# Performance work log

Measured on AMD Instinct MI355X. Metric: run time of the kernel, lower is better.

The kernel has to match this reference:

```python
import jax, jax.numpy as jnp
import numpy as np

DIM = 1024
N_SLOTS = 64
SCALE = 1.0 / np.sqrt(DIM).astype(np.float32)


def _orthogonal(key, n, scale):
    a = jax.random.normal(key, (n, n), dtype=jnp.float32)
    q, r = jnp.linalg.qr(a)
    q = q * jnp.sign(jnp.diag(r))[None, :]
    return q * scale


def setup_inputs() -> dict:
    key = jax.random.key(0)
    ks = jax.random.split(key, 8)
    B, T, D = 16, 1024, DIM
    s = 1.0 / np.sqrt(D)
    x = jax.random.normal(ks[0], (B, T, D), dtype=jnp.float32)
    in_proj_w = jax.random.uniform(ks[1], (D, D), minval=-s, maxval=s, dtype=jnp.float32)
    out_proj_w = jax.random.uniform(ks[2], (D, D), minval=-s, maxval=s, dtype=jnp.float32)
    gate_proj_w = jax.random.uniform(ks[3], (D, D), minval=-s, maxval=s, dtype=jnp.float32)
    W_x = jax.random.uniform(ks[4], (D, D), minval=-s, maxval=s, dtype=jnp.float32)
    W_h = _orthogonal(ks[5], D, 0.9)
    W_write = jax.random.uniform(ks[6], (D, D), minval=-s, maxval=s, dtype=jnp.float32)
    b_h = jnp.zeros((D,), dtype=jnp.float32)
    return {"x": x, "in_proj_w": in_proj_w, "out_proj_w": out_proj_w,
            "gate_proj_w": gate_proj_w, "W_x": W_x, "W_h": W_h,
            "W_write": W_write, "b_h": b_h}


def _cell(x_proj, W_x, W_h, W_write, b_h):
    # x_proj: [B, T, D]
    B, T, D = x_proj.shape
    wx_all = jnp.einsum('btd,ed->bte', x_proj, W_x)  # precomputed W_x @ x
    h_tape0 = jnp.zeros((B, N_SLOTS, D), dtype=x_proj.dtype)
    h_work0 = jnp.zeros((B, D), dtype=x_proj.dtype)

    def step(carry, wx_t):
        h_tape, h_work = carry
        Rh = h_work @ W_h.T
        read_attn = jax.nn.softmax(jnp.einsum('bd,bnd->bn', h_work, h_tape) * SCALE, axis=-1)
        read = jnp.einsum('bn,bnd->bd', read_attn, h_tape)
        h_work = jnp.tanh(Rh + wx_t + read + b_h)
        write_val = h_work @ W_write.T
        write_attn = jax.nn.softmax(jnp.einsum('bd,bnd->bn', h_work, h_tape) * SCALE, axis=-1)
        wa = write_attn[..., None]  # [B, N, 1]
        h_tape = (1.0 - wa) * h_tape + wa * write_val[:, None, :]
        return (h_tape, h_work), h_work

    (h_tape_f, h_work_f), h_work_all = jax.lax.scan(
        step, (h_tape0, h_work0), jnp.swapaxes(wx_all, 0, 1))
    return jnp.swapaxes(h_work_all, 0, 1), h_tape_f, h_work_f


def reference(x, in_proj_w, out_proj_w, gate_proj_w, W_x, W_h, W_write, b_h):
    x_proj = x @ in_proj_w.T  # [B, T, D]
    h_work_all, h_tape_f, h_work_f = _cell(x_proj, W_x, W_h, W_write, b_h)
    gate = jax.nn.silu(x @ gate_proj_w.T)
    output = (h_work_all * gate) @ out_proj_w.T
    return output, h_tape_f, h_work_f
```

## Files before the change

kernel.cpp:

```cpp
#include <hip/hip_runtime.h>
#include <math.h>

#define SCALE_F 0.03125f

template<bool BT, int EPI>
__global__ __launch_bounds__(256) void gemm_nt(const float* __restrict__ A,
                                               const float* __restrict__ Bm,
                                               float* __restrict__ C,
                                               int M, int N, int K) {
  __shared__ float As[32][68];
  __shared__ float Bs[32][68];
  const int tid = threadIdx.x;
  const int n0 = blockIdx.x * 64;
  const int m0 = blockIdx.y * 64;
  const int i0 = (tid >> 4) * 4;
  const int j0 = (tid & 15) * 4;
  float acc[4][4] = {};

  for (int k0 = 0; k0 < K; k0 += 32) {
#pragma unroll
    for (int s = 0; s < 2; ++s) {
      int id = tid + 256 * s;
      int r = id >> 3, c4 = id & 7;
      float4 v = *(const float4*)&A[(size_t)(m0 + r) * K + k0 + c4 * 4];
      As[c4 * 4 + 0][r] = v.x; As[c4 * 4 + 1][r] = v.y;
      As[c4 * 4 + 2][r] = v.z; As[c4 * 4 + 3][r] = v.w;
    }
    if (BT) {
#pragma unroll
      for (int s = 0; s < 2; ++s) {
        int id = tid + 256 * s;
        int r = id >> 3, c4 = id & 7;
        float4 v = *(const float4*)&Bm[(size_t)(n0 + r) * K + k0 + c4 * 4];
        Bs[c4 * 4 + 0][r] = v.x; Bs[c4 * 4 + 1][r] = v.y;
        Bs[c4 * 4 + 2][r] = v.z; Bs[c4 * 4 + 3][r] = v.w;
      }
    } else {
#pragma unroll
      for (int s = 0; s < 2; ++s) {
        int id = tid + 256 * s;
        int kk = id >> 4, c4 = id & 15;
        float4 v = *(const float4*)&Bm[(size_t)(k0 + kk) * N + n0 + c4 * 4];
        *(float4*)&Bs[kk][c4 * 4] = v;
      }
    }
    __syncthreads();
#pragma unroll
    for (int kk = 0; kk < 32; ++kk) {
      float4 a = *(const float4*)&As[kk][i0];
      float4 b = *(const float4*)&Bs[kk][j0];
      float av[4] = {a.x, a.y, a.z, a.w};
      float bv[4] = {b.x, b.y, b.z, b.w};
#pragma unroll
      for (int ii = 0; ii < 4; ++ii)
#pragma unroll
        for (int jj = 0; jj < 4; ++jj)
          acc[ii][jj] = fmaf(av[ii], bv[jj], acc[ii][jj]);
    }
    __syncthreads();
  }

#pragma unroll
  for (int ii = 0; ii < 4; ++ii) {
    float4 v;
    float* vp = (float*)&v;
#pragma unroll
    for (int jj = 0; jj < 4; ++jj) {
      float x = acc[ii][jj];
      if (EPI == 1) x = x / (1.0f + __expf(-x));
      vp[jj] = x;
    }
    *(float4*)&C[(size_t)(m0 + i0 + ii) * N + n0 + j0] = v;
  }
}

typedef unsigned long long u64;
__device__ __forceinline__ u64 ald64(const u64* p) {
  return __hip_atomic_load(p, __ATOMIC_RELAXED, __HIP_MEMORY_SCOPE_AGENT);
}
__device__ __forceinline__ void ast64(u64* p, u64 v) {
  __hip_atomic_store(p, v, __ATOMIC_RELAXED, __HIP_MEMORY_SCOPE_AGENT);
}
__device__ __forceinline__ u64 pk(float v, int j) {
  return ((u64)(unsigned)j << 32) | (u64)__float_as_uint(v);
}
__device__ __forceinline__ float pollv(const u64* p, int j) {
  u64 u = ald64(p);
  while ((unsigned)(u >> 32) != (unsigned)j) {
    __builtin_amdgcn_s_sleep(1);
    u = ald64(p);
  }
  return __uint_as_float((unsigned)u);
}

#define TIDX(n, e) ((n) * 64 + (((e) + (n)) & 63))

#define REP32(M) M(0) M(1) M(2) M(3) M(4) M(5) M(6) M(7) M(8) M(9) M(10) \
  M(11) M(12) M(13) M(14) M(15) M(16) M(17) M(18) M(19) M(20) M(21) M(22) \
  M(23) M(24) M(25) M(26) M(27) M(28) M(29) M(30) M(31)

#define RW(i) const float wh##i = Whp[32 * (i)]; \
              const float ww##i = Wwp[32 * (i)];
#define MVI(i) { float4 hh = ht4[cseg + 32 * (i)]; \
  ah0 = fmaf(wh##i, hh.x, ah0); ah1 = fmaf(wh##i, hh.y, ah1); \
  ah2 = fmaf(wh##i, hh.z, ah2); ah3 = fmaf(wh##i, hh.w, ah3); \
  aw0 = fmaf(ww##i, hh.x, aw0); aw1 = fmaf(ww##i, hh.y, aw1); \
  aw2 = fmaf(ww##i, hh.z, aw2); aw3 = fmaf(ww##i, hh.w, aw3); }

__global__ __launch_bounds__(512) void scan_kernel(
    const float* __restrict__ W_h, const float* __restrict__ W_wr,
    const float* __restrict__ b_h, const float* __restrict__ gate,
    float* __restrict__ wx,
    u64* __restrict__ h2,
    u64* __restrict__ ps2,
    u64* __restrict__ Rh2,
    u64* __restrict__ wv2,
    u64* __restrict__ qp2,
    float* __restrict__ hfin,
    float* __restrict__ tape_out)
{
  const int tid  = threadIdx.x;
  const int wg   = blockIdx.x;
  const int g    = wg >> 6;
  const int idx  = wg & 63;
  const int b_loc = idx >> 4;
  const int es   = idx & 15;
  const int gb   = g * 4;
  const int bsel = gb + b_loc;
  const int E0   = es * 64;
  const int R0   = es * 64 + b_loc * 16;
  const int w    = tid >> 6;
  const int lane = tid & 63;
  const int row  = tid >> 5;
  const int cseg = tid & 31;
  const int gr   = R0 + row;
  const int nwr  = tid >> 3;
  const int ksb  = tid & 7;

  __shared__ float h_t[4096];
  __shared__ float tape_l[4096];
  __shared__ float qtmp[16][4];
  __shared__ float ws_lds[64], wa_lds[64], attn_lds[64];
  __shared__ float wv_lds[64], Rh_lds[64], h_own[64], read_lds[64];
  __shared__ volatile float lds_pad[12288];
  lds_pad[tid] = 0.0f; lds_pad[tid + 512] = 0.0f;

  const float* Whp = W_h + (size_t)gr * 1024 + cseg;
  const float* Wwp = W_wr + (size_t)gr * 1024 + cseg;
  REP32(RW)

  const float4* ht4 = (const float4*)h_t;

  for (int i = tid; i < 4096; i += 512) tape_l[i] = 0.0f;

  float bh_r = 0.0f;
  if (w == 0) bh_r = b_h[E0 + lane];
  __syncthreads();

  if (w == 0) {
    size_t xi = (size_t)bsel * 1048576 + E0 + lane;
    float hv = tanhf(wx[xi] + bh_r);
    h_own[lane] = hv;
    ast64(&h2[(size_t)bsel * 1024 + E0 + lane], pk(hv, 1));
    wx[xi] = hv * gate[xi];
  }
  if (tid < 64) ast64(&ps2[(size_t)bsel * 1024 + es * 64 + tid], pk(0.0f, 1));
  __syncthreads();

  for (int j = 1; j <= 1024; ++j) {
    const bool last = (j == 1024);

#pragma unroll
    for (int r = 0; r < 8; ++r) {
      int i = tid + r * 512;
      int bl = i >> 10, d = i & 1023;
      h_t[4 * d + bl] = pollv(&h2[(size_t)(gb + bl) * 1024 + d], j);
    }
    float p0 = pollv(&ps2[(size_t)bsel * 1024 + (ksb * 2) * 64 + nwr], j);
    float p1 = pollv(&ps2[(size_t)bsel * 1024 + (ksb * 2 + 1) * 64 + nwr], j);
    float wxv = 0.0f, gv = 0.0f;
    size_t xj = 0;
    if (w == 0 && !last) {
      xj  = (size_t)bsel * 1048576 + (size_t)j * 1024 + E0 + lane;
      wxv = wx[xj];
      gv  = gate[xj];
    }
    __syncthreads();

    {
      float s = p0 + p1;
      s += __shfl_xor(s, 1);
      s += __shfl_xor(s, 2);
      s += __shfl_xor(s, 4);
      if (ksb == 0) ws_lds[nwr] = s;
    }
    float ah0 = 0.0f, ah1 = 0.0f, ah2 = 0.0f, ah3 = 0.0f;
    float aw0 = 0.0f, aw1 = 0.0f, aw2 = 0.0f, aw3 = 0.0f;
    REP32(MVI)
#pragma unroll
    for (int m = 1; m < 32; m <<= 1) {
      ah0 += __shfl_xor(ah0, m); ah1 += __shfl_xor(ah1, m);
      ah2 += __shfl_xor(ah2, m); ah3 += __shfl_xor(ah3, m);
      aw0 += __shfl_xor(aw0, m); aw1 += __shfl_xor(aw1, m);
      aw2 += __shfl_xor(aw2, m); aw3 += __shfl_xor(aw3, m);
    }
    if (cseg == 0) {
      ast64(&Rh2[(size_t)(gb + 0) * 1024 + gr], pk(ah0, j));
      ast64(&Rh2[(size_t)(gb + 1) * 1024 + gr], pk(ah1, j));
      ast64(&Rh2[(size_t)(gb + 2) * 1024 + gr], pk(ah2, j));
      ast64(&Rh2[(size_t)(gb + 3) * 1024 + gr], pk(ah3, j));
      ast64(&wv2[(size_t)(gb + 0) * 1024 + gr], pk(aw0, j));
      ast64(&wv2[(size_t)(gb + 1) * 1024 + gr], pk(aw1, j));
      ast64(&wv2[(size_t)(gb + 2) * 1024 + gr], pk(aw2, j));
      ast64(&wv2[(size_t)(gb + 3) * 1024 + gr], pk(aw3, j));
      qtmp[row][0] = aw0 * h_t[4 * gr + 0];
      qtmp[row][1] = aw1 * h_t[4 * gr + 1];
      qtmp[row][2] = aw2 * h_t[4 * gr + 2];
      qtmp[row][3] = aw3 * h_t[4 * gr + 3];
    }
    __syncthreads();

    if (w == 0) {
      float s = ws_lds[lane] * SCALE_F;
      float m = s;
#pragma unroll
      for (int off = 1; off < 64; off <<= 1) m = fmaxf(m, __shfl_xor(m, off));
      float ex = __expf(s - m);
      float sum = ex;
#pragma unroll
      for (int off = 1; off < 64; off <<= 1) sum += __shfl_xor(sum, off);
      wa_lds[lane] = ex / sum;
    } else if (w == 1) {
      int bq = lane >> 4, r = lane & 15;
      float s = qtmp[r][bq];
      s += __shfl_xor(s, 1); s += __shfl_xor(s, 2);
      s += __shfl_xor(s, 4); s += __shfl_xor(s, 8);
      if (r == 0) ast64(&qp2[(size_t)(gb + bq) * 64 + idx], pk(s, j));
      float qv = pollv(&qp2[(size_t)bsel * 64 + lane], j);
#pragma unroll
      for (int off = 1; off < 64; off <<= 1) qv += __shfl_xor(qv, off);
      if (!last) {
        float wsr = ws_lds[lane];
        float sm = wsr * SCALE_F;
        float m = sm;
#pragma unroll
        for (int off = 1; off < 64; off <<= 1) m = fmaxf(m, __shfl_xor(m, off));
        float ex = __expf(sm - m);
        float sum = ex;
#pragma unroll
        for (int off = 1; off < 64; off <<= 1) sum += __shfl_xor(sum, off);
        float wa_l = ex / sum;
        float rs = fmaf(wa_l, qv - wsr, wsr) * SCALE_F;
        float m2 = rs;
#pragma unroll
        for (int off = 1; off < 64; off <<= 1) m2 = fmaxf(m2, __shfl_xor(m2, off));
        float ex2 = __expf(rs - m2);
        float sum2 = ex2;
#pragma unroll
        for (int off = 1; off < 64; off <<= 1) sum2 += __shfl_xor(sum2, off);
        attn_lds[lane] = ex2 / sum2;
      }
    } else if (w == 2) {
      wv_lds[lane] = pollv(&wv2[(size_t)bsel * 1024 + E0 + lane], j);
    } else if (w == 3) {
      Rh_lds[lane] = pollv(&Rh2[(size_t)bsel * 1024 + E0 + lane], j);
    }
    __syncthreads();

    {
      float wa = wa_lds[nwr];
#pragma unroll
      for (int i = 0; i < 8; ++i) {
        int e = ksb * 8 + i;
        int ix = TIDX(nwr, e);
        float t = tape_l[ix];
        tape_l[ix] = fmaf(wa, wv_lds[e] - t, t);
      }
    }
    if (last) break;
    __syncthreads();

    {
      int ge = tid >> 3, gn = tid & 7;
      float gsum = 0.0f;
#pragma unroll
      for (int i = 0; i < 8; ++i) {
        int n = gn * 8 + i;
        gsum = fmaf(attn_lds[n], tape_l[TIDX(n, ge)], gsum);
      }
      gsum += __shfl_xor(gsum, 1);
      gsum += __shfl_xor(gsum, 2);
      gsum += __shfl_xor(gsum, 4);
      if (gn == 0) read_lds[ge] = gsum;
    }
    __syncthreads();

    if (w == 0) {
      float hv = tanhf(Rh_lds[lane] + wxv + read_lds[lane] + bh_r);
      h_own[lane] = hv;
      ast64(&h2[(size_t)bsel * 1024 + E0 + lane], pk(hv, j + 1));
      wx[xj] = hv * gv;
    }
    __syncthreads();

    {
      float s = 0.0f;
#pragma unroll
      for (int i = 0; i < 8; ++i) {
        int e = ksb * 8 + i;
        s = fmaf(h_own[e], tape_l[TIDX(nwr, e)], s);
      }
      s += __shfl_xor(s, 1);
      s += __shfl_xor(s, 2);
      s += __shfl_xor(s, 4);
      if (ksb == 0) ast64(&ps2[(size_t)bsel * 1024 + es * 64 + nwr], pk(s, j + 1));
    }
  }

#pragma unroll
  for (int i = 0; i < 8; ++i) {
    int e = ksb * 8 + i;
    tape_out[(size_t)(bsel * 64 + nwr) * 1024 + E0 + e] = tape_l[TIDX(nwr, e)];
  }
  if (w == 0) hfin[(size_t)bsel * 1024 + E0 + lane] = h_own[lane];
}

extern "C" void kernel_launch(void* const* d_in, const int* in_sizes, int n_in,
                              void* d_out, int out_size, void* d_ws, size_t ws_size,
                              hipStream_t stream) {
  (void)in_sizes; (void)n_in; (void)out_size; (void)ws_size;
  const float* x      = (const float*)d_in[0];
  const float* in_w   = (const float*)d_in[1];
  const float* out_w  = (const float*)d_in[2];
  const float* gate_w = (const float*)d_in[3];
  const float* W_x    = (const float*)d_in[4];
  const float* W_h    = (const float*)d_in[5];
  const float* W_wr   = (const float*)d_in[6];
  const float* b_h    = (const float*)d_in[7];

  float* out  = (float*)d_out;
  float* tape = out + (size_t)16 * 1024 * 1024;
  float* hfin = tape + (size_t)16 * 64 * 1024;

  float* ws = (float*)d_ws;
  u64* h2  = (u64*)ws;
  u64* ps2 = (u64*)(ws + 32768);
  u64* Rh2 = (u64*)(ws + 65536);
  u64* wv2 = (u64*)(ws + 98304);
  u64* qp2 = (u64*)(ws + 131072);
  float* M1 = ws;
  float* wx = ws + (1 << 20);

  float* gate = out;

  dim3 blk(256);
  gemm_nt<false, 0><<<dim3(16, 16), blk, 0, stream>>>(W_x, in_w, M1, 1024, 1024, 1024);
  gemm_nt<true, 1><<<dim3(16, 256), blk, 0, stream>>>(x, gate_w, gate, 16384, 1024, 1024);
  gemm_nt<true, 0><<<dim3(16, 256), blk, 0, stream>>>(x, M1, wx, 16384, 1024, 1024);
  hipMemsetAsync(ws, 0, 133120 * sizeof(float), stream);
  scan_kernel<<<256, 512, 0, stream>>>(W_h, W_wr, b_h, gate, wx, h2, ps2,
                                       Rh2, wv2, qp2, hfin, tape);
  gemm_nt<true, 0><<<dim3(16, 256), blk, 0, stream>>>(wx, out_w, out, 16384, 1024, 1024);
}
```

Measured before the change: 10.94 ms.

## Batch spin-poll loads and publish per-wave q partials to cut sync latency

Each thread's per-step polling of h and partial-score flags becomes one combined loop that issues all ten tagged loads together and retries only when some tag is stale. Before, eight separate poll loops ran one after another. The q partial products are now reduced per wave with shuffles and published directly to a larger global buffer (8 entries per workgroup). This removes the LDS qtmp staging, the extra reduction, and the serial publish-then-poll step inside wave 1, and wave 1 now polls 8 entries per lane. The cost is more global atomic traffic and a larger memset region.

Result: slower. 12.69 ms (+15.9%).

```diff
diff --git a/kernel.cpp b/kernel.cpp
--- a/kernel.cpp
+++ b/kernel.cpp
@@ -84,13 +84,16 @@
 __device__ __forceinline__ u64 pk(float v, int j) {
   return ((u64)(unsigned)j << 32) | (u64)__float_as_uint(v);
 }
+__device__ __forceinline__ float lo(u64 u) {
+  return __uint_as_float((unsigned)u);
+}
 __device__ __forceinline__ float pollv(const u64* p, int j) {
   u64 u = ald64(p);
   while ((unsigned)(u >> 32) != (unsigned)j) {
     __builtin_amdgcn_s_sleep(1);
     u = ald64(p);
   }
-  return __uint_as_float((unsigned)u);
+  return lo(u);
 }
 
 #define TIDX(n, e) ((n) * 64 + (((e) + (n)) & 63))
@@ -106,6 +109,8 @@
   ah2 = fmaf(wh##i, hh.z, ah2); ah3 = fmaf(wh##i, hh.w, ah3); \
   aw0 = fmaf(ww##i, hh.x, aw0); aw1 = fmaf(ww##i, hh.y, aw1); \
   aw2 = fmaf(ww##i, hh.z, aw2); aw3 = fmaf(ww##i, hh.w, aw3); }
+
+#define TAGOK(u) ((unsigned)((u) >> 32) == tj)
 
 __global__ __launch_bounds__(512) void scan_kernel(
     const float* __restrict__ W_h, const float* __restrict__ W_wr,
@@ -115,7 +120,7 @@
     u64* __restrict__ ps2,
     u64* __restrict__ Rh2,
     u64* __restrict__ wv2,
-    u64* __restrict__ qp2,
+    u64* __restrict__ qp2b,
     float* __restrict__ hfin,
     float* __restrict__ tape_out)
 {
@@ -139,7 +144,6 @@
 
   __shared__ float h_t[4096];
   __shared__ float tape_l[4096];
-  __shared__ float qtmp[16][4];
   __shared__ float ws_lds[64], wa_lds[64], attn_lds[64];
   __shared__ float wv_lds[64], Rh_lds[64], h_own[64], read_lds[64];
   __shared__ volatile float lds_pad[12288];
@@ -169,15 +173,30 @@
 
   for (int j = 1; j <= 1024; ++j) {
     const bool last = (j == 1024);
-
-#pragma unroll
-    for (int r = 0; r < 8; ++r) {
-      int i = tid + r * 512;
-      int bl = i >> 10, d = i & 1023;
-      h_t[4 * d + bl] = pollv(&h2[(size_t)(gb + bl) * 1024 + d], j);
-    }
-    float p0 = pollv(&ps2[(size_t)bsel * 1024 + (ksb * 2) * 64 + nwr], j);
-    float p1 = pollv(&ps2[(size_t)bsel * 1024 + (ksb * 2 + 1) * 64 + nwr], j);
+    const unsigned tj = (unsigned)j;
+
+    float p0, p1;
+    {
+      const int d0 = tid, d1 = tid + 512;
+      const u64* hp = &h2[(size_t)gb * 1024];
+      const u64* pA = &ps2[(size_t)bsel * 1024 + (ksb * 2) * 64 + nwr];
+      const u64* pB = &ps2[(size_t)bsel * 1024 + (ksb * 2 + 1) * 64 + nwr];
+      u64 a0, a1, a2, a3, c0, c1, c2, c3, u0, u1;
+      for (;;) {
+        a0 = ald64(hp + 0 * 1024 + d0); a1 = ald64(hp + 1 * 1024 + d0);
+        a2 = ald64(hp + 2 * 1024 + d0); a3 = ald64(hp + 3 * 1024 + d0);
+        c0 = ald64(hp + 0 * 1024 + d1); c1 = ald64(hp + 1 * 1024 + d1);
+        c2 = ald64(hp + 2 * 1024 + d1); c3 = ald64(hp + 3 * 1024 + d1);
+        u0 = ald64(pA); u1 = ald64(pB);
+        if (TAGOK(a0) && TAGOK(a1) && TAGOK(a2) && TAGOK(a3) &&
+            TAGOK(c0) && TAGOK(c1) && TAGOK(c2) && TAGOK(c3) &&
+            TAGOK(u0) && TAGOK(u1)) break;
+        __builtin_amdgcn_s_sleep(1);
+      }
+      ((float4*)h_t)[d0] = make_float4(lo(a0), lo(a1), lo(a2), lo(a3));
+      ((float4*)h_t)[d1] = make_float4(lo(c0), lo(c1), lo(c2), lo(c3));
+      p0 = lo(u0); p1 = lo(u1);
+    }
     float wxv = 0.0f, gv = 0.0f;
     size_t xj = 0;
     if (w == 0 && !last) {
@@ -203,6 +222,19 @@
       ah2 += __shfl_xor(ah2, m); ah3 += __shfl_xor(ah3, m);
       aw0 += __shfl_xor(aw0, m); aw1 += __shfl_xor(aw1, m);
       aw2 += __shfl_xor(aw2, m); aw3 += __shfl_xor(aw3, m);
+    }
+    {
+      float4 hrow = ht4[gr];
+      float t0 = aw0 * hrow.x, t1 = aw1 * hrow.y;
+      float t2 = aw2 * hrow.z, t3 = aw3 * hrow.w;
+      t0 += __shfl_xor(t0, 32); t1 += __shfl_xor(t1, 32);
+      t2 += __shfl_xor(t2, 32); t3 += __shfl_xor(t3, 32);
+      if (lane == 0) {
+        ast64(&qp2b[(size_t)(gb + 0) * 512 + idx * 8 + w], pk(t0, j));
+        ast64(&qp2b[(size_t)(gb + 1) * 512 + idx * 8 + w], pk(t1, j));
+        ast64(&qp2b[(size_t)(gb + 2) * 512 + idx * 8 + w], pk(t2, j));
+        ast64(&qp2b[(size_t)(gb + 3) * 512 + idx * 8 + w], pk(t3, j));
+      }
     }
     if (cseg == 0) {
       ast64(&Rh2[(size_t)(gb + 0) * 1024 + gr], pk(ah0, j));
@@ -213,10 +245,6 @@
       ast64(&wv2[(size_t)(gb + 1) * 1024 + gr], pk(aw1, j));
       ast64(&wv2[(size_t)(gb + 2) * 1024 + gr], pk(aw2, j));
       ast64(&wv2[(size_t)(gb + 3) * 1024 + gr], pk(aw3, j));
-      qtmp[row][0] = aw0 * h_t[4 * gr + 0];
-      qtmp[row][1] = aw1 * h_t[4 * gr + 1];
-      qtmp[row][2] = aw2 * h_t[4 * gr + 2];
-      qtmp[row][3] = aw3 * h_t[4 * gr + 3];
     }
     __syncthreads();
 
@@ -231,15 +259,21 @@
       for (int off = 1; off < 64; off <<= 1) sum += __shfl_xor(sum, off);
       wa_lds[lane] = ex / sum;
     } else if (w == 1) {
-      int bq = lane >> 4, r = lane & 15;
-      float s = qtmp[r][bq];
-      s += __shfl_xor(s, 1); s += __shfl_xor(s, 2);
-      s += __shfl_xor(s, 4); s += __shfl_xor(s, 8);
-      if (r == 0) ast64(&qp2[(size_t)(gb + bq) * 64 + idx], pk(s, j));
-      float qv = pollv(&qp2[(size_t)bsel * 64 + lane], j);
-#pragma unroll
-      for (int off = 1; off < 64; off <<= 1) qv += __shfl_xor(qv, off);
       if (!last) {
+        const u64* qb = &qp2b[(size_t)bsel * 512 + lane * 8];
+        u64 q0, q1, q2, q3, q4, q5, q6, q7;
+        for (;;) {
+          q0 = ald64(qb + 0); q1 = ald64(qb + 1); q2 = ald64(qb + 2);
+          q3 = ald64(qb + 3); q4 = ald64(qb + 4); q5 = ald64(qb + 5);
+          q6 = ald64(qb + 6); q7 = ald64(qb + 7);
+          if (TAGOK(q0) && TAGOK(q1) && TAGOK(q2) && TAGOK(q3) &&
+              TAGOK(q4) && TAGOK(q5) && TAGOK(q6) && TAGOK(q7)) break;
+          __builtin_amdgcn_s_sleep(1);
+        }
+        float qv = lo(q0) + lo(q1) + lo(q2) + lo(q3) +
+                   lo(q4) + lo(q5) + lo(q6) + lo(q7);
+#pragma unroll
+        for (int off = 1; off < 64; off <<= 1) qv += __shfl_xor(qv, off);
         float wsr = ws_lds[lane];
         float sm = wsr * SCALE_F;
         float m = sm;
@@ -343,11 +377,11 @@
   float* hfin = tape + (size_t)16 * 64 * 1024;
 
   float* ws = (float*)d_ws;
-  u64* h2  = (u64*)ws;
-  u64* ps2 = (u64*)(ws + 32768);
-  u64* Rh2 = (u64*)(ws + 65536);
-  u64* wv2 = (u64*)(ws + 98304);
-  u64* qp2 = (u64*)(ws + 131072);
+  u64* h2   = (u64*)ws;
+  u64* ps2  = (u64*)(ws + 32768);
+  u64* Rh2  = (u64*)(ws + 65536);
+  u64* wv2  = (u64*)(ws + 98304);
+  u64* qp2b = (u64*)(ws + 131072);
   float* M1 = ws;
   float* wx = ws + (1 << 20);
 
@@ -357,8 +391,8 @@
   gemm_nt<false, 0><<<dim3(16, 16), blk, 0, stream>>>(W_x, in_w, M1, 1024, 1024, 1024);
   gemm_nt<true, 1><<<dim3(16, 256), blk, 0, stream>>>(x, gate_w, gate, 16384, 1024, 1024);
   gemm_nt<true, 0><<<dim3(16, 256), blk, 0, stream>>>(x, M1, wx, 16384, 1024, 1024);
-  hipMemsetAsync(ws, 0, 133120 * sizeof(float), stream);
+  hipMemsetAsync(ws, 0, 147456 * sizeof(float), stream);
   scan_kernel<<<256, 512, 0, stream>>>(W_h, W_wr, b_h, gate, wx, h2, ps2,
-                                       Rh2, wv2, qp2, hfin, tape);
+                                       Rh2, wv2, qp2b, hfin, tape);
   gemm_nt<true, 0><<<dim3(16, 256), blk, 0, stream>>>(wx, out_w, out, 16384, 1024, 1024);
 }
```

## Batch flag polls, move q reduction off LDS, double-buffer tape to drop a barrier

Applied to the files above, without the earlier changes.

The scan kernel now issues all of its tagged atomic loads for h and partial scores before spinning on any of them, so the latencies overlap instead of each poll serialising. The q partials are reduced per wave with a shuffle and published to a wider qp2 array, which removes the qtmp LDS staging. The tape is double-buffered and the read is computed from the old tape plus an algebraic correction term (s2*write_val), which removes one __syncthreads per step and keeps the updated tape values in registers. The cost is a larger workspace memset, more global atomic traffic for q, and a longer sleep interval in the spin loop.

Result: slower. 13.49 ms (+23.3%).

```diff
diff --git a/kernel.cpp b/kernel.cpp
--- a/kernel.cpp
+++ b/kernel.cpp
@@ -84,13 +84,13 @@
 __device__ __forceinline__ u64 pk(float v, int j) {
   return ((u64)(unsigned)j << 32) | (u64)__float_as_uint(v);
 }
-__device__ __forceinline__ float pollv(const u64* p, int j) {
-  u64 u = ald64(p);
-  while ((unsigned)(u >> 32) != (unsigned)j) {
-    __builtin_amdgcn_s_sleep(1);
+__device__ __forceinline__ float lo(u64 u) { return __uint_as_float((unsigned)u); }
+__device__ __forceinline__ u64 fx(const u64* p, u64 u, unsigned tj) {
+  while ((unsigned)(u >> 32) != tj) {
+    __builtin_amdgcn_s_sleep(2);
     u = ald64(p);
   }
-  return __uint_as_float((unsigned)u);
+  return u;
 }
 
 #define TIDX(n, e) ((n) * 64 + (((e) + (n)) & 63))
@@ -138,12 +138,12 @@
   const int ksb  = tid & 7;
 
   __shared__ float h_t[4096];
-  __shared__ float tape_l[4096];
-  __shared__ float qtmp[16][4];
+  __shared__ float tape_l[2][4096];
   __shared__ float ws_lds[64], wa_lds[64], attn_lds[64];
   __shared__ float wv_lds[64], Rh_lds[64], h_own[64], read_lds[64];
-  __shared__ volatile float lds_pad[12288];
-  lds_pad[tid] = 0.0f; lds_pad[tid + 512] = 0.0f;
+  __shared__ float s2_lds;
+  __shared__ volatile float lds_pad[8192];
+  lds_pad[tid] = 0.0f; lds_pad[tid + 4096] = 0.0f;
 
   const float* Whp = W_h + (size_t)gr * 1024 + cseg;
   const float* Wwp = W_wr + (size_t)gr * 1024 + cseg;
@@ -151,7 +151,10 @@
 
   const float4* ht4 = (const float4*)h_t;
 
-  for (int i = tid; i < 4096; i += 512) tape_l[i] = 0.0f;
+  for (int i = tid; i < 4096; i += 512) {
+    tape_l[0][i] = 0.0f;
+    tape_l[1][i] = 0.0f;
+  }
 
   float bh_r = 0.0f;
   if (w == 0) bh_r = b_h[E0 + lane];
@@ -167,17 +170,13 @@
   if (tid < 64) ast64(&ps2[(size_t)bsel * 1024 + es * 64 + tid], pk(0.0f, 1));
   __syncthreads();
 
+  int cur = 0;
+  float t0, t1, t2, t3, t4, t5, t6, t7;
+
   for (int j = 1; j <= 1024; ++j) {
     const bool last = (j == 1024);
-
-#pragma unroll
-    for (int r = 0; r < 8; ++r) {
-      int i = tid + r * 512;
-      int bl = i >> 10, d = i & 1023;
-      h_t[4 * d + bl] = pollv(&h2[(size_t)(gb + bl) * 1024 + d], j);
-    }
-    float p0 = pollv(&ps2[(size_t)bsel * 1024 + (ksb * 2) * 64 + nwr], j);
-    float p1 = pollv(&ps2[(size_t)bsel * 1024 + (ksb * 2 + 1) * 64 + nwr], j);
+    const unsigned tj = (unsigned)j;
+
     float wxv = 0.0f, gv = 0.0f;
     size_t xj = 0;
     if (w == 0 && !last) {
@@ -185,15 +184,35 @@
       wxv = wx[xj];
       gv  = gate[xj];
     }
-    __syncthreads();
 
     {
-      float s = p0 + p1;
+      const u64* hb = h2 + (size_t)gb * 1024;
+      const u64 *pa0 = hb + 0 * 1024 + 2 * tid, *pa1 = hb + 0 * 1024 + 2 * tid + 1;
+      const u64 *pb0 = hb + 1 * 1024 + 2 * tid, *pb1 = hb + 1 * 1024 + 2 * tid + 1;
+      const u64 *pc0 = hb + 2 * 1024 + 2 * tid, *pc1 = hb + 2 * 1024 + 2 * tid + 1;
+      const u64 *pd0 = hb + 3 * 1024 + 2 * tid, *pd1 = hb + 3 * 1024 + 2 * tid + 1;
+      const u64 *pp0 = &ps2[(size_t)bsel * 1024 + (ksb * 2) * 64 + nwr];
+      const u64 *pp1 = &ps2[(size_t)bsel * 1024 + (ksb * 2 + 1) * 64 + nwr];
+      u64 a0 = ald64(pa0), a1 = ald64(pa1);
+      u64 b0 = ald64(pb0), b1 = ald64(pb1);
+      u64 c0 = ald64(pc0), c1 = ald64(pc1);
+      u64 d0 = ald64(pd0), d1 = ald64(pd1);
+      u64 u0 = ald64(pp0), u1 = ald64(pp1);
+      a0 = fx(pa0, a0, tj); a1 = fx(pa1, a1, tj);
+      b0 = fx(pb0, b0, tj); b1 = fx(pb1, b1, tj);
+      c0 = fx(pc0, c0, tj); c1 = fx(pc1, c1, tj);
+      d0 = fx(pd0, d0, tj); d1 = fx(pd1, d1, tj);
+      u0 = fx(pp0, u0, tj); u1 = fx(pp1, u1, tj);
+      ((float4*)h_t)[2 * tid]     = make_float4(lo(a0), lo(b0), lo(c0), lo(d0));
+      ((float4*)h_t)[2 * tid + 1] = make_float4(lo(a1), lo(b1), lo(c1), lo(d1));
+      float s = lo(u0) + lo(u1);
       s += __shfl_xor(s, 1);
       s += __shfl_xor(s, 2);
       s += __shfl_xor(s, 4);
       if (ksb == 0) ws_lds[nwr] = s;
     }
+    __syncthreads();
+
     float ah0 = 0.0f, ah1 = 0.0f, ah2 = 0.0f, ah3 = 0.0f;
     float aw0 = 0.0f, aw1 = 0.0f, aw2 = 0.0f, aw3 = 0.0f;
     REP32(MVI)
@@ -203,6 +222,19 @@
       ah2 += __shfl_xor(ah2, m); ah3 += __shfl_xor(ah3, m);
       aw0 += __shfl_xor(aw0, m); aw1 += __shfl_xor(aw1, m);
       aw2 += __shfl_xor(aw2, m); aw3 += __shfl_xor(aw3, m);
+    }
+    {
+      float4 hrow = ht4[gr];
+      float q0 = aw0 * hrow.x, q1 = aw1 * hrow.y;
+      float q2 = aw2 * hrow.z, q3 = aw3 * hrow.w;
+      q0 += __shfl_xor(q0, 32); q1 += __shfl_xor(q1, 32);
+      q2 += __shfl_xor(q2, 32); q3 += __shfl_xor(q3, 32);
+      if (lane == 0) {
+        ast64(&qp2[(size_t)(gb + 0) * 512 + idx * 8 + w], pk(q0, j));
+        ast64(&qp2[(size_t)(gb + 1) * 512 + idx * 8 + w], pk(q1, j));
+        ast64(&qp2[(size_t)(gb + 2) * 512 + idx * 8 + w], pk(q2, j));
+        ast64(&qp2[(size_t)(gb + 3) * 512 + idx * 8 + w], pk(q3, j));
+      }
     }
     if (cseg == 0) {
       ast64(&Rh2[(size_t)(gb + 0) * 1024 + gr], pk(ah0, j));
@@ -213,10 +245,6 @@
       ast64(&wv2[(size_t)(gb + 1) * 1024 + gr], pk(aw1, j));
       ast64(&wv2[(size_t)(gb + 2) * 1024 + gr], pk(aw2, j));
       ast64(&wv2[(size_t)(gb + 3) * 1024 + gr], pk(aw3, j));
-      qtmp[row][0] = aw0 * h_t[4 * gr + 0];
-      qtmp[row][1] = aw1 * h_t[4 * gr + 1];
-      qtmp[row][2] = aw2 * h_t[4 * gr + 2];
-      qtmp[row][3] = aw3 * h_t[4 * gr + 3];
     }
     __syncthreads();
 
@@ -231,14 +259,6 @@
       for (int off = 1; off < 64; off <<= 1) sum += __shfl_xor(sum, off);
       wa_lds[lane] = ex / sum;
     } else if (w == 1) {
-      int bq = lane >> 4, r = lane & 15;
-      float s = qtmp[r][bq];
-      s += __shfl_xor(s, 1); s += __shfl_xor(s, 2);
-      s += __shfl_xor(s, 4); s += __shfl_xor(s, 8);
-      if (r == 0) ast64(&qp2[(size_t)(gb + bq) * 64 + idx], pk(s, j));
-      float qv = pollv(&qp2[(size_t)bsel * 64 + lane], j);
-#pragma unroll
-      for (int off = 1; off < 64; off <<= 1) qv += __shfl_xor(qv, off);
       if (!last) {
         float wsr = ws_lds[lane];
         float sm = wsr * SCALE_F;
@@ -250,6 +270,18 @@
 #pragma unroll
         for (int off = 1; off < 64; off <<= 1) sum += __shfl_xor(sum, off);
         float wa_l = ex / sum;
+        const u64* qb = &qp2[(size_t)bsel * 512 + lane * 8];
+        u64 q0 = ald64(qb + 0), q1 = ald64(qb + 1), q2 = ald64(qb + 2),
+            q3 = ald64(qb + 3), q4 = ald64(qb + 4), q5 = ald64(qb + 5),
+            q6 = ald64(qb + 6), q7 = ald64(qb + 7);
+        q0 = fx(qb + 0, q0, tj); q1 = fx(qb + 1, q1, tj);
+        q2 = fx(qb + 2, q2, tj); q3 = fx(qb + 3, q3, tj);
+        q4 = fx(qb + 4, q4, tj); q5 = fx(qb + 5, q5, tj);
+        q6 = fx(qb + 6, q6, tj); q7 = fx(qb + 7, q7, tj);
+        float qv = lo(q0) + lo(q1) + lo(q2) + lo(q3) +
+                   lo(q4) + lo(q5) + lo(q6) + lo(q7);
+#pragma unroll
+        for (int off = 1; off < 64; off <<= 1) qv += __shfl_xor(qv, off);
         float rs = fmaf(wa_l, qv - wsr, wsr) * SCALE_F;
         float m2 = rs;
 #pragma unroll
@@ -258,41 +290,52 @@
         float sum2 = ex2;
 #pragma unroll
         for (int off = 1; off < 64; off <<= 1) sum2 += __shfl_xor(sum2, off);
-        attn_lds[lane] = ex2 / sum2;
+        float att = ex2 / sum2;
+        attn_lds[lane] = att * (1.0f - wa_l);
+        float s2 = att * wa_l;
+#pragma unroll
+        for (int off = 1; off < 64; off <<= 1) s2 += __shfl_xor(s2, off);
+        if (lane == 0) s2_lds = s2;
       }
     } else if (w == 2) {
-      wv_lds[lane] = pollv(&wv2[(size_t)bsel * 1024 + E0 + lane], j);
+      const u64* p = &wv2[(size_t)bsel * 1024 + E0 + lane];
+      u64 v = ald64(p);
+      v = fx(p, v, tj);
+      wv_lds[lane] = lo(v);
     } else if (w == 3) {
-      Rh_lds[lane] = pollv(&Rh2[(size_t)bsel * 1024 + E0 + lane], j);
-    }
-    __syncthreads();
-
-    {
-      float wa = wa_lds[nwr];
-#pragma unroll
-      for (int i = 0; i < 8; ++i) {
-        int e = ksb * 8 + i;
-        int ix = TIDX(nwr, e);
-        float t = tape_l[ix];
-        tape_l[ix] = fmaf(wa, wv_lds[e] - t, t);
-      }
-    }
-    if (last) break;
-    __syncthreads();
-
-    {
+      const u64* p = &Rh2[(size_t)bsel * 1024 + E0 + lane];
+      u64 v = ald64(p);
+      v = fx(p, v, tj);
+      Rh_lds[lane] = lo(v);
+    }
+    __syncthreads();
+
+    const float* tp_cur = tape_l[cur];
+    float* tp_nxt = tape_l[cur ^ 1];
+    if (!last) {
       int ge = tid >> 3, gn = tid & 7;
       float gsum = 0.0f;
 #pragma unroll
       for (int i = 0; i < 8; ++i) {
         int n = gn * 8 + i;
-        gsum = fmaf(attn_lds[n], tape_l[TIDX(n, ge)], gsum);
+        gsum = fmaf(attn_lds[n], tp_cur[TIDX(n, ge)], gsum);
       }
       gsum += __shfl_xor(gsum, 1);
       gsum += __shfl_xor(gsum, 2);
       gsum += __shfl_xor(gsum, 4);
-      if (gn == 0) read_lds[ge] = gsum;
-    }
+      if (gn == 0) read_lds[ge] = gsum + s2_lds * wv_lds[ge];
+    }
+    {
+      float wa = wa_lds[nwr];
+#define LERP(i, tr) { int e = ksb * 8 + (i); int ix = TIDX(nwr, e); \
+      float tv = tp_cur[ix]; tv = fmaf(wa, wv_lds[e] - tv, tv); \
+      tp_nxt[ix] = tv; tr = tv; }
+      LERP(0, t0) LERP(1, t1) LERP(2, t2) LERP(3, t3)
+      LERP(4, t4) LERP(5, t5) LERP(6, t6) LERP(7, t7)
+#undef LERP
+    }
+    cur ^= 1;
+    if (last) break;
     __syncthreads();
 
     if (w == 0) {
@@ -304,23 +347,24 @@
     __syncthreads();
 
     {
-      float s = 0.0f;
-#pragma unroll
-      for (int i = 0; i < 8; ++i) {
-        int e = ksb * 8 + i;
-        s = fmaf(h_own[e], tape_l[TIDX(nwr, e)], s);
-      }
+      float s = t0 * h_own[ksb * 8 + 0] + t1 * h_own[ksb * 8 + 1] +
+                t2 * h_own[ksb * 8 + 2] + t3 * h_own[ksb * 8 + 3] +
+                t4 * h_own[ksb * 8 + 4] + t5 * h_own[ksb * 8 + 5] +
+                t6 * h_own[ksb * 8 + 6] + t7 * h_own[ksb * 8 + 7];
       s += __shfl_xor(s, 1);
       s += __shfl_xor(s, 2);
       s += __shfl_xor(s, 4);
-      if (ksb == 0) ast64(&ps2[(size_t)bsel * 1024 + es * 64 + nwr], pk(s, j + 1));
-    }
-  }
-
-#pragma unroll
-  for (int i = 0; i < 8; ++i) {
-    int e = ksb * 8 + i;
-    tape_out[(size_t)(bsel * 64 + nwr) * 1024 + E0 + e] = tape_l[TIDX(nwr, e)];
+      if (ksb == 0)
+        ast64(&ps2[(size_t)bsel * 1024 + es * 64 + nwr], pk(s, j + 1));
+    }
+  }
+
+  {
+    float* dst = &tape_out[(size_t)(bsel * 64 + nwr) * 1024 + E0];
+    dst[ksb * 8 + 0] = t0; dst[ksb * 8 + 1] = t1;
+    dst[ksb * 8 + 2] = t2; dst[ksb * 8 + 3] = t3;
+    dst[ksb * 8 + 4] = t4; dst[ksb * 8 + 5] = t5;
+    dst[ksb * 8 + 6] = t6; dst[ksb * 8 + 7] = t7;
   }
   if (w == 0) hfin[(size_t)bsel * 1024 + E0 + lane] = h_own[lane];
 }
@@ -357,7 +401,7 @@
   gemm_nt<false, 0><<<dim3(16, 16), blk, 0, stream>>>(W_x, in_w, M1, 1024, 1024, 1024);
   gemm_nt<true, 1><<<dim3(16, 256), blk, 0, stream>>>(x, gate_w, gate, 16384, 1024, 1024);
   gemm_nt<true, 0><<<dim3(16, 256), blk, 0, stream>>>(x, M1, wx, 16384, 1024, 1024);
-  hipMemsetAsync(ws, 0, 133120 * sizeof(float), stream);
+  hipMemsetAsync(ws, 0, 147456 * sizeof(float), stream);
   scan_kernel<<<256, 512, 0, stream>>>(W_h, W_wr, b_h, gate, wx, h2, ps2,
                                        Rh2, wv2, qp2, hfin, tape);
   gemm_nt<true, 0><<<dim3(16, 256), blk, 0, stream>>>(wx, out_w, out, 16384, 1024, 1024);
```

## Batch flag polls, drop qtmp LDS reduction, remap workgroups across groups

Applied to the files above, without the earlier changes.

Issues all h and partial-sum atomic loads at once before spinning on each, so the load latency of a step overlaps instead of being serialized poll by poll. The write-attention dot product is now reduced per wave with a shuffle and published as eight partials per workgroup, removing the qtmp shared buffer and one reduction stage. The consumer wave polls and sums those partials. Block-to-group mapping is interleaved (g = wg & 3), which changes how groups spread across the chip, and the zeroed workspace grows to cover the larger qp buffer.

New measurement: 11.18 ms. 1.02x slower.

```diff
diff --git a/kernel.cpp b/kernel.cpp
--- a/kernel.cpp
+++ b/kernel.cpp
@@ -84,13 +84,21 @@
 __device__ __forceinline__ u64 pk(float v, int j) {
   return ((u64)(unsigned)j << 32) | (u64)__float_as_uint(v);
 }
+__device__ __forceinline__ float lo(u64 u) { return __uint_as_float((unsigned)u); }
 __device__ __forceinline__ float pollv(const u64* p, int j) {
   u64 u = ald64(p);
   while ((unsigned)(u >> 32) != (unsigned)j) {
     __builtin_amdgcn_s_sleep(1);
     u = ald64(p);
   }
-  return __uint_as_float((unsigned)u);
+  return lo(u);
+}
+__device__ __forceinline__ u64 fx(const u64* p, u64 u, unsigned tj) {
+  while ((unsigned)(u >> 32) != tj) {
+    __builtin_amdgcn_s_sleep(1);
+    u = ald64(p);
+  }
+  return u;
 }
 
 #define TIDX(n, e) ((n) * 64 + (((e) + (n)) & 63))
@@ -106,6 +114,8 @@
   ah2 = fmaf(wh##i, hh.z, ah2); ah3 = fmaf(wh##i, hh.w, ah3); \
   aw0 = fmaf(ww##i, hh.x, aw0); aw1 = fmaf(ww##i, hh.y, aw1); \
   aw2 = fmaf(ww##i, hh.z, aw2); aw3 = fmaf(ww##i, hh.w, aw3); }
+
+#define TAGOK(u) ((unsigned)((u) >> 32) == tj)
 
 __global__ __launch_bounds__(512) void scan_kernel(
     const float* __restrict__ W_h, const float* __restrict__ W_wr,
@@ -121,8 +131,8 @@
 {
   const int tid  = threadIdx.x;
   const int wg   = blockIdx.x;
-  const int g    = wg >> 6;
-  const int idx  = wg & 63;
+  const int g    = wg & 3;
+  const int idx  = wg >> 2;
   const int b_loc = idx >> 4;
   const int es   = idx & 15;
   const int gb   = g * 4;
@@ -139,7 +149,6 @@
 
   __shared__ float h_t[4096];
   __shared__ float tape_l[4096];
-  __shared__ float qtmp[16][4];
   __shared__ float ws_lds[64], wa_lds[64], attn_lds[64];
   __shared__ float wv_lds[64], Rh_lds[64], h_own[64], read_lds[64];
   __shared__ volatile float lds_pad[12288];
@@ -169,15 +178,8 @@
 
   for (int j = 1; j <= 1024; ++j) {
     const bool last = (j == 1024);
-
-#pragma unroll
-    for (int r = 0; r < 8; ++r) {
-      int i = tid + r * 512;
-      int bl = i >> 10, d = i & 1023;
-      h_t[4 * d + bl] = pollv(&h2[(size_t)(gb + bl) * 1024 + d], j);
-    }
-    float p0 = pollv(&ps2[(size_t)bsel * 1024 + (ksb * 2) * 64 + nwr], j);
-    float p1 = pollv(&ps2[(size_t)bsel * 1024 + (ksb * 2 + 1) * 64 + nwr], j);
+    const unsigned tj = (unsigned)j;
+
     float wxv = 0.0f, gv = 0.0f;
     size_t xj = 0;
     if (w == 0 && !last) {
@@ -185,15 +187,35 @@
       wxv = wx[xj];
       gv  = gate[xj];
     }
-    __syncthreads();
-
-    {
-      float s = p0 + p1;
+
+    {
+      const u64* hb = h2 + (size_t)gb * 1024;
+      const u64 *pa0 = hb + 0 * 1024 + 2 * tid, *pa1 = pa0 + 1;
+      const u64 *pb0 = hb + 1 * 1024 + 2 * tid, *pb1 = pb0 + 1;
+      const u64 *pc0 = hb + 2 * 1024 + 2 * tid, *pc1 = pc0 + 1;
+      const u64 *pd0 = hb + 3 * 1024 + 2 * tid, *pd1 = pd0 + 1;
+      const u64 *pp0 = &ps2[(size_t)bsel * 1024 + (ksb * 2) * 64 + nwr];
+      const u64 *pp1 = &ps2[(size_t)bsel * 1024 + (ksb * 2 + 1) * 64 + nwr];
+      u64 a0 = ald64(pa0), a1 = ald64(pa1);
+      u64 b0 = ald64(pb0), b1 = ald64(pb1);
+      u64 c0 = ald64(pc0), c1 = ald64(pc1);
+      u64 d0 = ald64(pd0), d1 = ald64(pd1);
+      u64 u0 = ald64(pp0), u1 = ald64(pp1);
+      a0 = fx(pa0, a0, tj); a1 = fx(pa1, a1, tj);
+      b0 = fx(pb0, b0, tj); b1 = fx(pb1, b1, tj);
+      c0 = fx(pc0, c0, tj); c1 = fx(pc1, c1, tj);
+      d0 = fx(pd0, d0, tj); d1 = fx(pd1, d1, tj);
+      u0 = fx(pp0, u0, tj); u1 = fx(pp1, u1, tj);
+      ((float4*)h_t)[2 * tid]     = make_float4(lo(a0), lo(b0), lo(c0), lo(d0));
+      ((float4*)h_t)[2 * tid + 1] = make_float4(lo(a1), lo(b1), lo(c1), lo(d1));
+      float s = lo(u0) + lo(u1);
       s += __shfl_xor(s, 1);
       s += __shfl_xor(s, 2);
       s += __shfl_xor(s, 4);
       if (ksb == 0) ws_lds[nwr] = s;
     }
+    __syncthreads();
+
     float ah0 = 0.0f, ah1 = 0.0f, ah2 = 0.0f, ah3 = 0.0f;
     float aw0 = 0.0f, aw1 = 0.0f, aw2 = 0.0f, aw3 = 0.0f;
     REP32(MVI)
@@ -213,10 +235,19 @@
       ast64(&wv2[(size_t)(gb + 1) * 1024 + gr], pk(aw1, j));
       ast64(&wv2[(size_t)(gb + 2) * 1024 + gr], pk(aw2, j));
       ast64(&wv2[(size_t)(gb + 3) * 1024 + gr], pk(aw3, j));
-      qtmp[row][0] = aw0 * h_t[4 * gr + 0];
-      qtmp[row][1] = aw1 * h_t[4 * gr + 1];
-      qtmp[row][2] = aw2 * h_t[4 * gr + 2];
-      qtmp[row][3] = aw3 * h_t[4 * gr + 3];
+    }
+    {
+      float4 hrow = ht4[gr];
+      float q0 = aw0 * hrow.x, q1 = aw1 * hrow.y;
+      float q2 = aw2 * hrow.z, q3 = aw3 * hrow.w;
+      q0 += __shfl_xor(q0, 32); q1 += __shfl_xor(q1, 32);
+      q2 += __shfl_xor(q2, 32); q3 += __shfl_xor(q3, 32);
+      if (lane == 0) {
+        ast64(&qp2[(size_t)(gb + 0) * 512 + idx * 8 + w], pk(q0, j));
+        ast64(&qp2[(size_t)(gb + 1) * 512 + idx * 8 + w], pk(q1, j));
+        ast64(&qp2[(size_t)(gb + 2) * 512 + idx * 8 + w], pk(q2, j));
+        ast64(&qp2[(size_t)(gb + 3) * 512 + idx * 8 + w], pk(q3, j));
+      }
     }
     __syncthreads();
 
@@ -231,14 +262,6 @@
       for (int off = 1; off < 64; off <<= 1) sum += __shfl_xor(sum, off);
       wa_lds[lane] = ex / sum;
     } else if (w == 1) {
-      int bq = lane >> 4, r = lane & 15;
-      float s = qtmp[r][bq];
-      s += __shfl_xor(s, 1); s += __shfl_xor(s, 2);
-      s += __shfl_xor(s, 4); s += __shfl_xor(s, 8);
-      if (r == 0) ast64(&qp2[(size_t)(gb + bq) * 64 + idx], pk(s, j));
-      float qv = pollv(&qp2[(size_t)bsel * 64 + lane], j);
-#pragma unroll
-      for (int off = 1; off < 64; off <<= 1) qv += __shfl_xor(qv, off);
       if (!last) {
         float wsr = ws_lds[lane];
         float sm = wsr * SCALE_F;
@@ -250,6 +273,13 @@
 #pragma unroll
         for (int off = 1; off < 64; off <<= 1) sum += __shfl_xor(sum, off);
         float wa_l = ex / sum;
+        const u64* qb = &qp2[(size_t)bsel * 512 + lane * 8];
+        float qv = pollv(qb + 0, j) + pollv(qb + 1, j) +
+                   pollv(qb + 2, j) + pollv(qb + 3, j) +
+                   pollv(qb + 4, j) + pollv(qb + 5, j) +
+                   pollv(qb + 6, j) + pollv(qb + 7, j);
+#pragma unroll
+        for (int off = 1; off < 64; off <<= 1) qv += __shfl_xor(qv, off);
         float rs = fmaf(wa_l, qv - wsr, wsr) * SCALE_F;
         float m2 = rs;
 #pragma unroll
@@ -313,7 +343,8 @@
       s += __shfl_xor(s, 1);
       s += __shfl_xor(s, 2);
       s += __shfl_xor(s, 4);
-      if (ksb == 0) ast64(&ps2[(size_t)bsel * 1024 + es * 64 + nwr], pk(s, j + 1));
+      if (ksb == 0)
+        ast64(&ps2[(size_t)bsel * 1024 + es * 64 + nwr], pk(s, j + 1));
     }
   }
 
@@ -357,7 +388,7 @@
   gemm_nt<false, 0><<<dim3(16, 16), blk, 0, stream>>>(W_x, in_w, M1, 1024, 1024, 1024);
   gemm_nt<true, 1><<<dim3(16, 256), blk, 0, stream>>>(x, gate_w, gate, 16384, 1024, 1024);
   gemm_nt<true, 0><<<dim3(16, 256), blk, 0, stream>>>(x, M1, wx, 16384, 1024, 1024);
-  hipMemsetAsync(ws, 0, 133120 * sizeof(float), stream);
+  hipMemsetAsync(ws, 0, 147456 * sizeof(float), stream);
   scan_kernel<<<256, 512, 0, stream>>>(W_h, W_wr, b_h, gate, wx, h2, ps2,
                                        Rh2, wv2, qp2, hfin, tape);
   gemm_nt<true, 0><<<dim3(16, 256), blk, 0, stream>>>(wx, out_w, out, 16384, 1024, 1024);
```
